# Kernel tuning notes

Measured on AMD Instinct MI355X. Metric: run time of the kernel, lower is better.

## Reference

```python
import jax, jax.numpy as jnp
import numpy as np

NEG = 0.01  # leaky_relu negative slope used throughout AttentiveFP


def _seg_softmax(logits, seg, num):
    # softmax over entries grouped by segment id (PyG softmax w/ 1e-16 eps)
    m = jax.ops.segment_max(logits, seg, num_segments=num)
    m = jnp.where(jnp.isfinite(m), m, 0.0)
    e = jnp.exp(logits - m[seg])
    s = jax.ops.segment_sum(e, seg, num_segments=num)
    return e / (s[seg] + 1e-16)


def _gru(x, h, wi, wh, bi, bh):
    # torch.nn.GRUCell math
    gi = x @ wi.T + bi
    gh = h @ wh.T + bh
    ir, iz, inn = jnp.split(gi, 3, axis=-1)
    hr, hz, hn = jnp.split(gh, 3, axis=-1)
    r = jax.nn.sigmoid(ir + hr)
    z = jax.nn.sigmoid(iz + hz)
    n = jnp.tanh(inn + r * hn)
    return (1.0 - z) * n + z * h


def _forward(x, edge_attr, mol_feats, lin1_w, lin1_b, gate_lin1_w, gate_lin2_w, gate_att_l, gate_att_r, gate_bias, grus_wi, grus_wh, grus_bi, grus_bh, atom_w, atom_att_src, atom_att_dst, atom_bias, mol_w, mol_att_src, mol_att_dst, mol_bias, lin2_w, lin2_b, fcm0_w, fcm0_b, fcm1_w, fcm1_b, fcm2_w, fcm2_b, fc0_w, fc0_b, fc1_w, fc1_b, fc2_w, fc2_b, fc3_w, fc3_b, fc4_w, fc4_b, edge_index, batch):
    N = x.shape[0]
    G = mol_feats.shape[0]
    src, dst = edge_index[0], edge_index[1]
    lrelu = lambda v: jax.nn.leaky_relu(v, NEG)
    # AttentiveFP (eval mode: dropout off)
    xh = lrelu(x @ lin1_w.T + lin1_b)  # [N,H]
    # --- GATEConv: edge-conditioned attention, add aggregation ---
    m = lrelu(jnp.concatenate([xh[src], edge_attr], axis=-1) @ gate_lin1_w.T)  # [E,H]
    a = lrelu(m @ gate_att_l + (xh @ gate_att_r)[dst])
    a = _seg_softmax(a, dst, N)
    h = jax.ops.segment_sum((m @ gate_lin2_w.T) * a[:, None], dst, num_segments=N) + gate_bias
    xh = jax.nn.relu(_gru(jax.nn.elu(h), xh, grus_wi[0], grus_wh[0], grus_bi[0], grus_bh[0]))
    # --- GATConv layers (num_layers-1 = 2, heads=1, no self loops) ---
    for l in range(2):
        xl = xh @ atom_w[l].T
        a = lrelu((xl @ atom_att_src[l])[src] + (xl @ atom_att_dst[l])[dst])
        a = _seg_softmax(a, dst, N)
        h = jax.ops.segment_sum(xl[src] * a[:, None], dst, num_segments=N) + atom_bias[l]
        xh = jax.nn.relu(_gru(jax.nn.elu(h), xh, grus_wi[1 + l], grus_wh[1 + l], grus_bi[1 + l], grus_bh[1 + l]))
    # --- attentive graph readout (num_timesteps = 3) ---
    out = jax.nn.relu(jax.ops.segment_sum(xh, batch, num_segments=G))  # [G,H]
    xm = xh @ mol_w.T            # atom-side lin (x fixed across timesteps)
    a_src = xm @ mol_att_src
    for _ in range(3):
        a = lrelu(a_src + ((out @ mol_w.T) @ mol_att_dst)[batch])
        a = _seg_softmax(a, batch, G)
        h = jax.ops.segment_sum(xm * a[:, None], batch, num_segments=G) + mol_bias
        out = jax.nn.relu(_gru(jax.nn.elu(h), out, grus_wi[3], grus_wh[3], grus_bi[3], grus_bh[3]))
    hg = out @ lin2_w.T + lin2_b  # [G,256]
    # --- mol-feature MLP branch (SiLU) ---
    hm = jax.nn.silu(mol_feats @ fcm0_w.T + fcm0_b)
    hm = jax.nn.silu(hm @ fcm1_w.T + fcm1_b)
    hm = jax.nn.silu(hm @ fcm2_w.T + fcm2_b)
    # --- fusion MLP ---
    hg = jnp.concatenate([hg, hm], axis=1)  # [G,512]
    hg = jax.nn.silu(hg @ fc0_w.T + fc0_b)
    hg = jax.nn.silu(hg @ fc1_w.T + fc1_b)
    hg = jax.nn.silu(hg @ fc2_w.T + fc2_b)
    hg = jax.nn.silu(hg @ fc3_w.T + fc3_b)
    return hg @ fc4_w.T + fc4_b  # [G,1]


def setup_inputs() -> dict:
    key = jax.random.key(0)
    ks = iter(jax.random.split(key, 64))
    def W(*shape):
        return jax.random.normal(next(ks), shape, jnp.float32) / np.float32(np.sqrt(shape[-1]))
    def B(*shape):
        return 0.02 * jax.random.normal(next(ks), shape, jnp.float32)
    N, E, G = 131072, 262144, 8192
    Fn, Fe, Fm, H = 64, 16, 200, 256
    return dict(
        x=jax.random.normal(next(ks), (N, Fn), jnp.float32),
        edge_attr=jax.random.normal(next(ks), (E, Fe), jnp.float32),
        mol_feats=jax.random.normal(next(ks), (G, Fm), jnp.float32),
        lin1_w=W(H, Fn), lin1_b=B(H),
        gate_lin1_w=W(H, H + Fe), gate_lin2_w=W(H, H),
        gate_att_l=W(H), gate_att_r=W(H), gate_bias=B(H),
        grus_wi=W(4, 3 * H, H), grus_wh=W(4, 3 * H, H), grus_bi=B(4, 3 * H), grus_bh=B(4, 3 * H),
        atom_w=W(2, H, H), atom_att_src=W(2, H), atom_att_dst=W(2, H), atom_bias=B(2, H),
        mol_w=W(H, H), mol_att_src=W(H), mol_att_dst=W(H), mol_bias=B(H),
        lin2_w=W(H, H), lin2_b=B(H),
        fcm0_w=W(H, Fm), fcm0_b=B(H), fcm1_w=W(H, H), fcm1_b=B(H), fcm2_w=W(H, H), fcm2_b=B(H),
        fc0_w=W(512, 512), fc0_b=B(512), fc1_w=W(512, 512), fc1_b=B(512),
        fc2_w=W(512, 512), fc2_b=B(512), fc3_w=W(128, 512), fc3_b=B(128),
        fc4_w=W(1, 128), fc4_b=B(1),
        edge_index=jax.random.randint(next(ks), (2, E), 0, N),
        batch=jnp.sort(jax.random.randint(next(ks), (N,), 0, G)),
    )


def reference(x, edge_attr, mol_feats, lin1_w, lin1_b, gate_lin1_w, gate_lin2_w, gate_att_l, gate_att_r, gate_bias, grus_wi, grus_wh, grus_bi, grus_bh, atom_w, atom_att_src, atom_att_dst, atom_bias, mol_w, mol_att_src, mol_att_dst, mol_bias, lin2_w, lin2_b, fcm0_w, fcm0_b, fcm1_w, fcm1_b, fcm2_w, fcm2_b, fc0_w, fc0_b, fc1_w, fc1_b, fc2_w, fc2_b, fc3_w, fc3_b, fc4_w, fc4_b, edge_index, batch):
    return _forward(x, edge_attr, mol_feats, lin1_w, lin1_b, gate_lin1_w, gate_lin2_w, gate_att_l, gate_att_r, gate_bias, grus_wi, grus_wh, grus_bi, grus_bh, atom_w, atom_att_src, atom_att_dst, atom_bias, mol_w, mol_att_src, mol_att_dst, mol_bias, lin2_w, lin2_b, fcm0_w, fcm0_b, fcm1_w, fcm1_b, fcm2_w, fcm2_b, fc0_w, fc0_b, fc1_w, fc1_b, fc2_w, fc2_b, fc3_w, fc3_b, fc4_w, fc4_b, edge_index, batch)
```

## Files before the change

### kernel.cpp

```cpp
#include <hip/hip_runtime.h>
#include <hip/hip_bf16.h>
#include <math.h>


typedef unsigned short u16;
typedef u16 u16x8 __attribute__((ext_vector_type(8)));
typedef short s16x8 __attribute__((ext_vector_type(8)));
typedef float f32x4 __attribute__((ext_vector_type(4)));

__device__ __forceinline__ float u2f(u16 u) { return __uint_as_float(((unsigned)u) << 16); }
__device__ __forceinline__ u16 f2u(float f) {
    return __builtin_bit_cast(u16, __float2bfloat16(f));
}

#define NEGS 0.01f

typedef const __attribute__((address_space(1))) unsigned gas1_t;
typedef __attribute__((address_space(3))) unsigned las3_t;
__device__ __forceinline__ void gload16(const void* g, void* l) {
    __builtin_amdgcn_global_load_lds((gas1_t*)g, (las3_t*)l, 16, 0, 0);
}

__device__ __forceinline__ unsigned fkey(float f) {
    unsigned u = __float_as_uint(f);
    return (u & 0x80000000u) ? ~u : (u | 0x80000000u);
}
__device__ __forceinline__ float funkey(unsigned k) {
    return (k & 0x80000000u) ? __uint_as_float(k ^ 0x80000000u) : __uint_as_float(~k);
}
#define KEY_NEG_INF 0x007FFFFFu

static inline int cdiv(int a, int b) { return (a + b - 1) / b; }

__global__ void fill_f32(float* p, float v, size_t n) {
    size_t i = (size_t)blockIdx.x * 256 + threadIdx.x;
    if (i < n) p[i] = v;
}
__global__ void fill_u32(unsigned* p, unsigned v, int n) {
    int i = blockIdx.x * 256 + threadIdx.x;
    if (i < n) p[i] = v;
}
__global__ void fill_km(unsigned* key, float* sum, int n) {
    int i = blockIdx.x * 256 + threadIdx.x;
    if (i < n) { key[i] = KEY_NEG_INF; sum[i] = 0.f; }
}
__global__ void copy_f2b(const float* s, u16* d, size_t n) {
    size_t i = (size_t)blockIdx.x * 256 + threadIdx.x;
    if (i < n) d[i] = f2u(s[i]);
}
__global__ void matvecT_k(const float* W, const float* a, float* v, int K, int Jout) {
    int j = blockIdx.x * 256 + threadIdx.x;
    if (j >= Jout) return;
    float s = 0.f;
    for (int k = 0; k < K; k++) s += W[(size_t)k * Jout + j] * a[k];
    v[j] = s;
}
__global__ void matvecT2_k(const float* W1, const float* a1, float* o1,
                           const float* W2, const float* a2, float* o2,
                           int K, int Jout) {
    int j = blockIdx.x * 256 + threadIdx.x;
    if (j < Jout) {
        float s = 0.f;
        for (int k = 0; k < K; k++) s += W1[(size_t)k * Jout + j] * a1[k];
        o1[j] = s;
    } else if (j < 2 * Jout) {
        int jj = j - Jout;
        float s = 0.f;
        for (int k = 0; k < K; k++) s += W2[(size_t)k * Jout + jj] * a2[k];
        o2[jj] = s;
    }
}
__global__ void edge_add_lrelu_max(const float* dp4, float* elog, const float* r,
                                   const int* dsti, unsigned* key, int E) {
    int i = blockIdx.x * 256 + threadIdx.x;
    if (i < E) {
        int d = dsti[i];
        float p = (dp4[i] + dp4[(size_t)E + i]) +
                  (dp4[(size_t)2 * E + i] + dp4[(size_t)3 * E + i]);
        float v = p + r[d];
        v = v > 0.f ? v : NEGS * v;
        elog[i] = v;
        atomicMax(&key[d], fkey(v));
    }
}
__global__ void pair_logit_max(float* elog, const float* s, const float* dd,
                               const int* srci, const int* dsti, unsigned* key, int E) {
    int i = blockIdx.x * 256 + threadIdx.x;
    if (i < E) {
        int d = dsti[i];
        float v = s[srci[i]] + dd[d];
        v = v > 0.f ? v : NEGS * v;
        elog[i] = v;
        atomicMax(&key[d], fkey(v));
    }
}
__global__ void node_logit_max(float* nlog, const float* asrc, const float* wg,
                               const int* batch, unsigned* key, int N) {
    int i = blockIdx.x * 256 + threadIdx.x;
    if (i < N) {
        int b = batch[i];
        float v = asrc[i] + wg[b];
        v = v > 0.f ? v : NEGS * v;
        nlog[i] = v;
        atomicMax(&key[b], fkey(v));
    }
}
__global__ void seg_exp_k(const float* logit, const int* idx, const unsigned* key,
                          float* ex, float* sum, int n) {
    int i = blockIdx.x * 256 + threadIdx.x;
    if (i < n) {
        float e = expf(logit[i] - funkey(key[idx[i]]));
        ex[i] = e;
        atomicAdd(&sum[idx[i]], e);
    }
}
__global__ void rowdot2_b(const u16* X, const float* v1, const float* v2,
                          float* o1, float* o2, int M) {
    int r = blockIdx.x * 4 + (threadIdx.x >> 6);
    int lane = threadIdx.x & 63;
    if (r >= M) return;
    ushort4 rv = *(const ushort4*)(X + (size_t)r * 256 + lane * 4);
    u16 q4[4] = {rv.x, rv.y, rv.z, rv.w};
    float p1 = 0.f, p2 = 0.f;
#pragma unroll
    for (int q = 0; q < 4; q++) {
        float xv = u2f(q4[q]);
        p1 += xv * v1[lane * 4 + q];
        if (v2) p2 += xv * v2[lane * 4 + q];
    }
    for (int off = 32; off; off >>= 1) {
        p1 += __shfl_down(p1, off);
        if (v2) p2 += __shfl_down(p2, off);
    }
    if (lane == 0) {
        o1[r] = p1;
        if (v2) o2[r] = p2;
    }
}
__global__ void rowdot_f(const float* X, const float* v1, float* o1, int M) {
    int r = blockIdx.x * 4 + (threadIdx.x >> 6);
    int lane = threadIdx.x & 63;
    if (r >= M) return;
    float4 a = ((const float4*)(X + (size_t)r * 256))[lane];
    float4 b = ((const float4*)v1)[lane];
    float p1 = a.x * b.x + a.y * b.y + a.z * b.z + a.w * b.w;
    for (int off = 32; off; off >>= 1) p1 += __shfl_down(p1, off);
    if (lane == 0) o1[r] = p1;
}
__global__ void fc4_k(const float* X, const float* w, const float* b, float* out, int G) {
    int g = blockIdx.x * 4 + (threadIdx.x >> 6);
    int lane = threadIdx.x & 63;
    if (g >= G) return;
    float2 xv = ((const float2*)(X + (size_t)g * 128))[lane];
    float2 wv = ((const float2*)w)[lane];
    float p = xv.x * wv.x + xv.y * wv.y;
    for (int off = 32; off; off >>= 1) p += __shfl_down(p, off);
    if (lane == 0) out[g] = p + b[0];
}

__global__ void count_dst(const int* dst, int* cnt, int E) {
    int i = blockIdx.x * 256 + threadIdx.x;
    if (i < E) atomicAdd(&cnt[dst[i]], 1);
}
__global__ void scan1(const int* cnt, int* part, int N) {
    __shared__ int sm[256];
    int i = blockIdx.x * 256 + threadIdx.x;
    sm[threadIdx.x] = i < N ? cnt[i] : 0;
    __syncthreads();
    for (int off = 128; off; off >>= 1) {
        if (threadIdx.x < off) sm[threadIdx.x] += sm[threadIdx.x + off];
        __syncthreads();
    }
    if (threadIdx.x == 0) part[blockIdx.x] = sm[0];
}
__global__ void scan2(int* part, int nb) {
    __shared__ int a[1024], b[1024];
    int t = threadIdx.x;
    if (nb > 1024) {
        if (t == 0) {
            int acc = 0;
            for (int i = 0; i < nb; i++) { int v = part[i]; part[i] = acc; acc += v; }
        }
        return;
    }
    int v = t < nb ? part[t] : 0;
    a[t] = v;
    __syncthreads();
    int* cur = a; int* nxt = b;
    for (int off = 1; off < 1024; off <<= 1) {
        int s = cur[t] + (t >= off ? cur[t - off] : 0);
        nxt[t] = s;
        __syncthreads();
        int* tmp = cur; cur = nxt; nxt = tmp;
    }
    if (t < nb) part[t] = cur[t] - v;
}
__global__ void scan3(const int* cnt, const int* part, int* rowstart, int N) {
    __shared__ int a[256], b[256];
    int t = threadIdx.x;
    int i = blockIdx.x * 256 + t;
    int v = i < N ? cnt[i] : 0;
    a[t] = v;
    __syncthreads();
    int* cur = a; int* nxt = b;
    for (int off = 1; off < 256; off <<= 1) {
        int s = cur[t] + (t >= off ? cur[t - off] : 0);
        nxt[t] = s;
        __syncthreads();
        int* tmp = cur; cur = nxt; nxt = tmp;
    }
    if (i < N) rowstart[i] = part[blockIdx.x] + cur[t] - v;
}
__global__ void fill_csr(const int* dst, const int* rowstart, int* fillc,
                         int* eorder, int E) {
    int e = blockIdx.x * 256 + threadIdx.x;
    if (e >= E) return;
    int d = dst[e];
    int s = rowstart[d] + atomicAdd(&fillc[d], 1);
    eorder[s] = e;
}
__global__ void chunk_dlo_k(const int* rowstart, const int* cnt, int N, int Crows,
                            int nch, int* dlo) {
    int c = blockIdx.x * 64 + threadIdx.x;
    if (c >= nch) return;
    int s0 = c * Crows;
    int lo = 0, hi = N;
    while (lo < hi) {
        int mid = (lo + hi) >> 1;
        if (rowstart[mid] + cnt[mid] > s0) hi = mid; else lo = mid + 1;
    }
    dlo[c] = lo;
}
template <int MODE>
__global__ void csr_red(const int* rowstart, const int* cnt, const int* eorder,
                        const float* ex, const float* sum, const int* srcE,
                        const u16* X, const u16* X2, int msplit,
                        int s0, int s1, const int* dlo,
                        u16* outH, u16* outL, int N) {
    int d;
    if (MODE == 1) {
        d = dlo[0] + blockIdx.x;
        if (d >= N) return;
        if (rowstart[d] >= s1) return;
    } else {
        d = blockIdx.x;
        if (d >= N) return;
    }
    int rs = rowstart[d], k = cnt[d];
    int lo = rs, hi = rs + k;
    if (MODE == 1) {
        if (lo < s0) lo = s0;
        if (hi > s1) hi = s1;
        if (lo >= hi) return;
    }
    float den = sum[d] + 1e-16f;
    int c = threadIdx.x;
    float acc = 0.f;
    for (int s = lo; s < hi; s++) {
        int e = eorder[s];
        float av = ex[e] / den;
        const u16* row;
        if (MODE == 0) row = X + (size_t)srcE[e] * 256;
        else if (MODE == 1) row = X + (size_t)(s - s0) * 256;
        else row = (e < msplit) ? X + (size_t)e * 256 : X2 + (size_t)(e - msplit) * 256;
        acc += av * u2f(row[c]);
    }
    size_t o = (size_t)d * 256 + c;
    if (MODE == 1) acc += u2f(outH[o]) + u2f(outL[o]);
    u16 hh = f2u(acc);
    outH[o] = hh;
    outL[o] = f2u(acc - u2f(hh));
}
__global__ void graph_bounds(const int* batch, int* gs, int* ge, int N) {
    int i = blockIdx.x * 256 + threadIdx.x;
    if (i >= N) return;
    int b = batch[i];
    atomicMin(&gs[b], i);
    atomicMax(&ge[b], i + 1);
}
template <bool RELU>
__global__ void seg_red(const int* gs, const int* ge, const u16* X, const float* sc,
                        const float* sum, float* out, int G) {
    int g = blockIdx.x;
    if (g >= G) return;
    int c = threadIdx.x;
    int s = gs[g], e = ge[g];
    float den = sc ? (sum[g] + 1e-16f) : 1.f;
    float acc = 0.f;
    if (s < e)
        for (int i = s; i < e; i++) {
            float v = u2f(X[(size_t)i * 256 + c]);
            if (sc) v *= sc[i] / den;
            acc += v;
        }
    out[(size_t)g * 256 + c] = RELU ? fmaxf(acc, 0.f) : acc;
}

__global__ void pack_w(const float* s1, const float* s2, int K1, int Ksrc,
                       int Nout, int Kp, u16* dst) {
    int idx = blockIdx.x * 256 + threadIdx.x;
    int kiters = Kp >> 5;
    int total = (Nout >> 7) * kiters * 512;
    if (idx >= total) return;
    int c = idx & 511;
    int rest = idx >> 9;
    int ki = rest % kiters, nb = rest / kiters;
    int n = (nb << 7) + (((c >> 6) & 7) << 4) + (c & 15);
    int k0 = (ki << 5) + (((c >> 4) & 3) << 3);
    u16x8 vh, vl;
#pragma unroll
    for (int j = 0; j < 8; j++) {
        int k = k0 + j;
        float f = 0.f;
        if (k < K1) f = s1[(size_t)n * K1 + k];
        else if (k < Ksrc) f = s2[(size_t)n * (Ksrc - K1) + (k - K1)];
        u16 h = f2u(f);
        vh[j] = h;
        vl[j] = f2u(f - u2f(h));
    }
    ((u16x8*)dst)[idx] = vh;
    ((u16x8*)dst)[idx + total] = vl;
}
__global__ void pack_gru_w(const float* wi, const float* wh, u16* dst) {
    int idx = blockIdx.x * 256 + threadIdx.x;
    const int total = 8 * 16 * 512;
    if (idx >= total) return;
    int c = idx & 511, rest = idx >> 9;
    int ki = rest & 15, nb = rest >> 4;
    int n = (nb << 7) + (((c >> 6) & 7) << 4) + (c & 15);
    int k0 = (ki << 5) + (((c >> 4) & 3) << 3);
    int grp = n >> 6, sub = (n >> 4) & 3, ch = grp * 16 + (n & 15);
    u16x8 vh, vl;
#pragma unroll
    for (int j = 0; j < 8; j++) {
        int k = k0 + j;
        float f;
        if (sub < 3) {
            int srow = sub * 256 + ch;
            f = (k < 256) ? wi[(size_t)srow * 256 + k]
                          : wh[(size_t)srow * 256 + (k - 256)];
        } else {
            f = (k < 256) ? 0.f : wh[(size_t)(512 + ch) * 256 + (k - 256)];
        }
        u16 h = f2u(f);
        vh[j] = h;
        vl[j] = f2u(f - u2f(h));
    }
    ((u16x8*)dst)[idx] = vh;
    ((u16x8*)dst)[idx + total] = vl;
}
__global__ void pack_gru_b(const float* bi, const float* bh, float* bp) {
    int n = blockIdx.x * 256 + threadIdx.x;
    if (n >= 1024) return;
    int grp = n >> 6, sub = (n >> 4) & 3, ch = grp * 16 + (n & 15);
    float v;
    if (sub == 0) v = bi[ch] + bh[ch];
    else if (sub == 1) v = bi[256 + ch] + bh[256 + ch];
    else if (sub == 2) v = bi[512 + ch] + bh[512 + ch];
    else v = bh[512 + ch];
    bp[n] = v;
}

struct p8 { u16x8 hi, lo; };
__device__ __forceinline__ u16x8 zero8() {
    u16x8 z;
#pragma unroll
    for (int j = 0; j < 8; j++) z[j] = 0;
    return z;
}
__device__ __forceinline__ p8 sp_zero() { p8 r; r.hi = zero8(); r.lo = zero8(); return r; }
__device__ __forceinline__ p8 sp_b(const u16* p) {
    p8 r;
    r.hi = *(const u16x8*)p;
    r.lo = zero8();
    return r;
}
__device__ __forceinline__ p8 sp_f(const float* p) {
    p8 r;
#pragma unroll
    for (int j = 0; j < 8; j++) {
        float x = p[j];
        u16 h = f2u(x);
        r.hi[j] = h;
        r.lo[j] = f2u(x - u2f(h));
    }
    return r;
}
__device__ __forceinline__ p8 sp_eluf(const float* p) {
    p8 r;
#pragma unroll
    for (int j = 0; j < 8; j++) {
        float x = p[j];
        float e = x > 0.f ? x : expm1f(x);
        u16 h = f2u(e);
        r.hi[j] = h;
        r.lo[j] = f2u(e - u2f(h));
    }
    return r;
}
template <int ALD>
__device__ __forceinline__ p8 ldA(bool valid, int k, int Ksrc, const u16* ab,
                                  const float* af, const float* x2) {
    if (!valid) return sp_zero();
    if (ALD == 1) {
        if (k >= Ksrc) return sp_zero();
        return sp_f(af + k);
    }
    if (ALD == 2 || ALD == 7) {
        if (k < 256) return sp_b(ab + k);
        if (k < 272) return sp_f(x2 + (k - 256));
        return sp_zero();
    }
    if (k < 256) return sp_eluf(af + k);
    return sp_f(x2 + (k - 256));
}
template <int ALD>
__device__ __forceinline__ bool lo_zero(int ki) {
    if (ALD == 2 || ALD == 7) return ki < 8;
    return false;
}
template <int ACT>
__device__ __forceinline__ float actf(float v) {
    if (ACT == 1) return v > 0.f ? v : NEGS * v;
    if (ACT == 3) return v / (1.f + expf(-v));
    return v;
}

template <int ALD, int ACT, int EPI>
__global__ __launch_bounds__(256, 4) void mgemm(
    int M, int Kp, int Ksrc,
    const float* Af, int lda, const u16* Ab, const u16* Ab2,
    const int* gidx, const float* X2f, const u16* Wp, const float* b1,
    float* Cf, u16* Cb, u16* Cb2, int csplit, int ldc,
    const float* attv, float* dotout, const int* didx) {
    __shared__ u16x8 lsAll[2048];
    u16x8* lsAh = lsAll;
    u16x8* lsAl = lsAll + 512;
    u16x8* lsWh = lsAll + 1024;
    u16x8* lsWl = lsAll + 1536;
    const int t = threadIdx.x;
    const int m0 = blockIdx.x * 128;
    const int nb = blockIdx.y;
    const int kiters = Kp >> 5;
    const int r0 = ((t >> 6) << 4) | (t & 15);
    const int kq = ((t >> 4) & 3) << 3;
    const int mA[2] = {m0 + r0, m0 + r0 + 64};
    const u16* abh[2]; const u16* abl[2];
    const float* afr[2]; const float* x2r[2];
    bool val[2];
#pragma unroll
    for (int h = 0; h < 2; h++) {
        int m = mA[h];
        val[h] = (m < M);
        int ms = val[h] ? m : 0;
        abh[h] = nullptr; abl[h] = nullptr; afr[h] = nullptr; x2r[h] = nullptr;
        if constexpr (ALD == 1) {
            afr[h] = Af + (size_t)ms * lda;
        } else if constexpr (ALD == 2) {
            abh[h] = Ab + (size_t)gidx[ms] * 256;
            x2r[h] = X2f + (size_t)ms * 16;
        } else if constexpr (ALD == 7) {
            int e = gidx[ms];
            abh[h] = Ab + (size_t)didx[e] * 256;
            x2r[h] = X2f + (size_t)e * 16;
        } else {
            abh[h] = Ab + (size_t)ms * 256;
            abl[h] = Ab2 + (size_t)ms * 256;
        }
    }
    const int wave = t >> 6, lane = t & 63;
    const int wm = (wave >> 1) << 6, wn = (wave & 1) << 6;
    f32x4 acc[4][4];
#pragma unroll
    for (int i = 0; i < 4; i++)
#pragma unroll
        for (int j = 0; j < 4; j++) {
            acc[i][j][0] = 0.f; acc[i][j][1] = 0.f; acc[i][j][2] = 0.f; acc[i][j][3] = 0.f;
        }
    const u16x8* wh0 = (const u16x8*)Wp + ((size_t)nb * kiters << 9);
    const u16x8* wl0 = wh0 + ((size_t)gridDim.y * kiters << 9);
    for (int ki = 0; ki < kiters; ki++) {
        int kb = (ki << 5) + kq;
        if constexpr (ALD == 6) {
            gload16(abh[0] + kb, &lsAh[t]);
            gload16(abh[1] + kb, &lsAh[t + 256]);
            gload16(abl[0] + kb, &lsAl[t]);
            gload16(abl[1] + kb, &lsAl[t + 256]);
        } else {
            p8 a0 = ldA<ALD>(val[0], kb, Ksrc, abh[0], afr[0], x2r[0]);
            p8 a1 = ldA<ALD>(val[1], kb, Ksrc, abh[1], afr[1], x2r[1]);
            lsAh[t] = a0.hi; lsAl[t] = a0.lo;
            lsAh[t + 256] = a1.hi; lsAl[t + 256] = a1.lo;
        }
        const u16x8* wsh = wh0 + ((size_t)ki << 9);
        const u16x8* wsl = wl0 + ((size_t)ki << 9);
        gload16(wsh + t, &lsWh[t]);
        gload16(wsh + t + 256, &lsWh[t + 256]);
        gload16(wsl + t, &lsWl[t]);
        gload16(wsl + t + 256, &lsWl[t + 256]);
        __syncthreads();
        s16x8 ah[4], al[4], wh[4], wl[4];
#pragma unroll
        for (int f = 0; f < 4; f++) {
            int ai = ((wm >> 4) + f) * 64 + lane;
            int wi = ((wn >> 4) + f) * 64 + lane;
            ah[f] = __builtin_bit_cast(s16x8, lsAh[ai]);
            al[f] = __builtin_bit_cast(s16x8, lsAl[ai]);
            wh[f] = __builtin_bit_cast(s16x8, lsWh[wi]);
            wl[f] = __builtin_bit_cast(s16x8, lsWl[wi]);
        }
        bool skip_lh = lo_zero<ALD>(ki);
#pragma unroll
        for (int fi = 0; fi < 4; fi++)
#pragma unroll
            for (int fj = 0; fj < 4; fj++) {
                acc[fi][fj] = __builtin_amdgcn_mfma_f32_16x16x32_bf16(
                    ah[fi], wh[fj], acc[fi][fj], 0, 0, 0);
                if (!skip_lh)
                    acc[fi][fj] = __builtin_amdgcn_mfma_f32_16x16x32_bf16(
                        al[fi], wh[fj], acc[fi][fj], 0, 0, 0);
                acc[fi][fj] = __builtin_amdgcn_mfma_f32_16x16x32_bf16(
                    ah[fi], wl[fj], acc[fi][fj], 0, 0, 0);
            }
        __syncthreads();
    }
    const int col = lane & 15, quad = lane >> 4;
    const int n_base = nb * 128 + wn;
    u16* lt = (u16*)lsAll;
    const int rowsM = M - m0;
    if constexpr (EPI == 2) {
        float dp[4][4] = {};
#pragma unroll
        for (int fi = 0; fi < 4; fi++)
#pragma unroll
            for (int fj = 0; fj < 4; fj++) {
                int nn = n_base + fj * 16 + col;
                float av = attv[nn];
#pragma unroll
                for (int r = 0; r < 4; r++) {
                    float v = actf<ACT>(acc[fi][fj][r]);
                    dp[fi][r] += v * av;
                    if (Cb) {
                        int lr = wm + fi * 16 + quad * 4 + r;
                        int lc = wn + fj * 16 + col;
                        lt[lr * 128 + lc] = f2u(v);
                    }
                }
            }
        const size_t slot = (size_t)(nb * 2 + (wn >> 6)) * (size_t)M;
#pragma unroll
        for (int fi = 0; fi < 4; fi++)
#pragma unroll
            for (int r = 0; r < 4; r++) {
                float p = dp[fi][r];
                p += __shfl_down(p, 8);
                p += __shfl_down(p, 4);
                p += __shfl_down(p, 2);
                p += __shfl_down(p, 1);
                int mm = m0 + wm + fi * 16 + quad * 4 + r;
                if (col == 0 && mm < M) dotout[slot + mm] = p;
            }
        if (Cb) {
            __syncthreads();
#pragma unroll
            for (int it = 0; it < 8; it++) {
                int idx = it * 256 + t;
                int row = idx >> 4, c8 = idx & 15;
                if (row < rowsM) {
                    int mm = m0 + row;
                    u16* dst = (mm < csplit) ? Cb + (size_t)mm * 256
                                             : Cb2 + (size_t)(mm - csplit) * 256;
                    ((u16x8*)(dst + nb * 128))[c8] = ((u16x8*)lt)[idx];
                }
            }
        }
    } else if constexpr (EPI == 4) {
#pragma unroll
        for (int fj = 0; fj < 4; fj++) {
            int nn = n_base + fj * 16 + col;
            float bb = b1 ? b1[nn] : 0.f;
#pragma unroll
            for (int fi = 0; fi < 4; fi++)
#pragma unroll
                for (int r = 0; r < 4; r++) {
                    float v = acc[fi][fj][r] + bb;
                    float e = v > 0.f ? v : expm1f(v);
                    int lr = wm + fi * 16 + quad * 4 + r;
                    int lc = wn + fj * 16 + col;
                    lt[lr * 128 + lc] = f2u(e);
                }
        }
        __syncthreads();
#pragma unroll
        for (int it = 0; it < 8; it++) {
            int idx = it * 256 + t;
            int row = idx >> 4, c8 = idx & 15;
            if (row < rowsM)
                ((u16x8*)(Cb + (size_t)(m0 + row) * ldc + nb * 128))[c8] =
                    ((u16x8*)lt)[idx];
        }
        __syncthreads();
#pragma unroll
        for (int fj = 0; fj < 4; fj++) {
            int nn = n_base + fj * 16 + col;
            float bb = b1 ? b1[nn] : 0.f;
#pragma unroll
            for (int fi = 0; fi < 4; fi++)
#pragma unroll
                for (int r = 0; r < 4; r++) {
                    float v = acc[fi][fj][r] + bb;
                    float e = v > 0.f ? v : expm1f(v);
                    u16 hh = f2u(e);
                    int lr = wm + fi * 16 + quad * 4 + r;
                    int lc = wn + fj * 16 + col;
                    lt[lr * 128 + lc] = f2u(e - u2f(hh));
                }
        }
        __syncthreads();
#pragma unroll
        for (int it = 0; it < 8; it++) {
            int idx = it * 256 + t;
            int row = idx >> 4, c8 = idx & 15;
            if (row < rowsM)
                ((u16x8*)(Cb2 + (size_t)(m0 + row) * ldc + nb * 128))[c8] =
                    ((u16x8*)lt)[idx];
        }
    } else if constexpr (EPI == 1) {
#pragma unroll
        for (int fj = 0; fj < 4; fj++) {
            int nn = n_base + fj * 16 + col;
            float bb = b1 ? b1[nn] : 0.f;
#pragma unroll
            for (int fi = 0; fi < 4; fi++)
#pragma unroll
                for (int r = 0; r < 4; r++) {
                    float v = actf<ACT>(acc[fi][fj][r] + bb);
                    int lr = wm + fi * 16 + quad * 4 + r;
                    int lc = wn + fj * 16 + col;
                    lt[lr * 128 + lc] = f2u(v);
                }
        }
        __syncthreads();
#pragma unroll
        for (int it = 0; it < 8; it++) {
            int idx = it * 256 + t;
            int row = idx >> 4, c8 = idx & 15;
            if (row < rowsM)
                ((u16x8*)(Cb + (size_t)(m0 + row) * ldc + nb * 128))[c8] =
                    ((u16x8*)lt)[idx];
        }
    } else {
#pragma unroll
        for (int fj = 0; fj < 4; fj++) {
            int nn = n_base + fj * 16 + col;
            float bb = b1 ? b1[nn] : 0.f;
#pragma unroll
            for (int fi = 0; fi < 4; fi++)
#pragma unroll
                for (int r = 0; r < 4; r++) {
                    int mm = m0 + wm + fi * 16 + quad * 4 + r;
                    if (mm >= M) continue;
                    float v = actf<ACT>(acc[fi][fj][r] + bb);
                    Cf[(size_t)mm * ldc + nn] = v;
                }
        }
    }
}

template <int ALD, bool HB, bool OB>
__global__ __launch_bounds__(256, 4) void mgemm_gru(
    int M, const float* Af, const u16* Ab, const u16* Ab2, const float* X2f,
    const u16* Wp, const float* bp, const u16* hb, const float* hf,
    float* of, u16* ob) {
    __shared__ u16x8 lsAll[2048];
    u16x8* lsAh = lsAll;
    u16x8* lsAl = lsAll + 512;
    u16x8* lsWh = lsAll + 1024;
    u16x8* lsWl = lsAll + 1536;
    const int t = threadIdx.x;
    const int m0 = blockIdx.x * 128;
    const int nb = blockIdx.y;
    const int r0 = ((t >> 6) << 4) | (t & 15);
    const int kq = ((t >> 4) & 3) << 3;
    const int mA[2] = {m0 + r0, m0 + r0 + 64};
    const u16* ehr[2]; const u16* elr[2]; const u16* xhr[2];
    const float* afr[2]; const float* x2r[2];
    bool val[2];
#pragma unroll
    for (int h = 0; h < 2; h++) {
        int m = mA[h];
        val[h] = (m < M);
        int ms = val[h] ? m : 0;
        ehr[h] = nullptr; elr[h] = nullptr; xhr[h] = nullptr;
        afr[h] = nullptr; x2r[h] = nullptr;
        if constexpr (ALD == 5) {
            ehr[h] = Ab + (size_t)ms * 256;
            elr[h] = Ab2 + (size_t)ms * 256;
            xhr[h] = hb + (size_t)ms * 256;
        } else {
            afr[h] = Af + (size_t)ms * 256;
            x2r[h] = X2f + (size_t)ms * 256;
        }
    }
    const int wave = t >> 6, lane = t & 63;
    const int wm = (wave >> 1) << 6, wn = (wave & 1) << 6;
    f32x4 acc[4][4];
#pragma unroll
    for (int i = 0; i < 4; i++)
#pragma unroll
        for (int j = 0; j < 4; j++) {
            acc[i][j][0] = 0.f; acc[i][j][1] = 0.f; acc[i][j][2] = 0.f; acc[i][j][3] = 0.f;
        }
    const u16x8* wh0 = (const u16x8*)Wp + ((size_t)nb * 16 << 9);
    const u16x8* wl0 = (const u16x8*)Wp + (size_t)(8 * 16 * 512) + ((size_t)nb * 16 << 9);
    for (int ki = 0; ki < 16; ki++) {
        int kb = (ki << 5) + kq;
        if constexpr (ALD == 5) {
            const u16* p0 = kb < 256 ? ehr[0] + kb : xhr[0] + (kb - 256);
            const u16* p1 = kb < 256 ? ehr[1] + kb : xhr[1] + (kb - 256);
            gload16(p0, &lsAh[t]);
            gload16(p1, &lsAh[t + 256]);
            if (ki < 8) {
                gload16(elr[0] + kb, &lsAl[t]);
                gload16(elr[1] + kb, &lsAl[t + 256]);
            }
        } else {
            p8 a0 = ldA<4>(val[0], kb, 512, nullptr, afr[0], x2r[0]);
            p8 a1 = ldA<4>(val[1], kb, 512, nullptr, afr[1], x2r[1]);
            lsAh[t] = a0.hi; lsAl[t] = a0.lo;
            lsAh[t + 256] = a1.hi; lsAl[t + 256] = a1.lo;
        }
        const u16x8* wsh = wh0 + ((size_t)ki << 9);
        const u16x8* wsl = wl0 + ((size_t)ki << 9);
        gload16(wsh + t, &lsWh[t]);
        gload16(wsh + t + 256, &lsWh[t + 256]);
        gload16(wsl + t, &lsWl[t]);
        gload16(wsl + t + 256, &lsWl[t + 256]);
        __syncthreads();
        s16x8 ah[4], al[4], wh[4], wl[4];
#pragma unroll
        for (int f = 0; f < 4; f++) {
            int ai = ((wm >> 4) + f) * 64 + lane;
            int wi = ((wn >> 4) + f) * 64 + lane;
            ah[f] = __builtin_bit_cast(s16x8, lsAh[ai]);
            al[f] = __builtin_bit_cast(s16x8, lsAl[ai]);
            wh[f] = __builtin_bit_cast(s16x8, lsWh[wi]);
            wl[f] = __builtin_bit_cast(s16x8, lsWl[wi]);
        }
        bool skip_lh = (ALD == 5) ? (ki >= 8) : false;
        bool hn_zero = (ki < 8);
#pragma unroll
        for (int fi = 0; fi < 4; fi++)
#pragma unroll
            for (int fj = 0; fj < 4; fj++) {
                if (fj == 3 && hn_zero) continue;
                acc[fi][fj] = __builtin_amdgcn_mfma_f32_16x16x32_bf16(
                    ah[fi], wh[fj], acc[fi][fj], 0, 0, 0);
                if (!skip_lh)
                    acc[fi][fj] = __builtin_amdgcn_mfma_f32_16x16x32_bf16(
                        al[fi], wh[fj], acc[fi][fj], 0, 0, 0);
                acc[fi][fj] = __builtin_amdgcn_mfma_f32_16x16x32_bf16(
                    ah[fi], wl[fj], acc[fi][fj], 0, 0, 0);
            }
        __syncthreads();
    }
    const int col = lane & 15, quad = lane >> 4;
    const int nbase = nb * 128 + wn;
    float br = bp[nbase + col];
    float bz = bp[nbase + 16 + col];
    float bn = bp[nbase + 32 + col];
    float bhn = bp[nbase + 48 + col];
    int ch = (nb * 2 + (wn >> 6)) * 16 + col;
    int lc = ((wn >> 6) << 4) + col;
    u16* lt = (u16*)lsAll;
    float* ft = (float*)lsAll;
#pragma unroll
    for (int fi = 0; fi < 4; fi++)
#pragma unroll
        for (int r = 0; r < 4; r++) {
            int m = m0 + wm + fi * 16 + quad * 4 + r;
            if (m >= M) continue;
            float rs = acc[fi][0][r] + br;
            float zs = acc[fi][1][r] + bz;
            float nsv = acc[fi][2][r] + bn;
            float hnv = acc[fi][3][r] + bhn;
            float rr = 1.f / (1.f + expf(-rs));
            float zz = 1.f / (1.f + expf(-zs));
            float nn = tanhf(nsv - hnv + rr * hnv);
            float ho = HB ? u2f(hb[(size_t)m * 256 + ch]) : hf[(size_t)m * 256 + ch];
            float o = fmaxf((1.f - zz) * nn + zz * ho, 0.f);
            int lr = wm + fi * 16 + quad * 4 + r;
            if (OB) lt[lr * 32 + lc] = f2u(o);
            else ft[lr * 32 + lc] = o;
        }
    __syncthreads();
    const int rowsM = M - m0;
    if (OB) {
#pragma unroll
        for (int it = 0; it < 2; it++) {
            int idx = it * 256 + t;
            int row = idx >> 2, c8 = idx & 3;
            if (row < rowsM)
                ((u16x8*)(ob + (size_t)(m0 + row) * 256 + nb * 32))[c8] =
                    ((u16x8*)lt)[idx];
        }
    } else {
#pragma unroll
        for (int it = 0; it < 4; it++) {
            int idx = it * 256 + t;
            int row = idx >> 3, c4 = idx & 7;
            if (row < rowsM)
                ((float4*)(of + (size_t)(m0 + row) * 256 + nb * 32))[c4] =
                    ((float4*)ft)[idx];
        }
    }
}

extern "C" void kernel_launch(void* const* d_in, const int* in_sizes, int n_in,
                              void* d_out, int out_size, void* d_ws, size_t ws_size,
                              hipStream_t stream) {
    const float* x = (const float*)d_in[0];
    const float* edge_attr = (const float*)d_in[1];
    const float* mol_feats = (const float*)d_in[2];
    const float* lin1_w = (const float*)d_in[3];
    const float* lin1_b = (const float*)d_in[4];
    const float* gate_lin1_w = (const float*)d_in[5];
    const float* gate_lin2_w = (const float*)d_in[6];
    const float* gate_att_l = (const float*)d_in[7];
    const float* gate_att_r = (const float*)d_in[8];
    const float* gate_bias = (const float*)d_in[9];
    const float* grus_wi = (const float*)d_in[10];
    const float* grus_wh = (const float*)d_in[11];
    const float* grus_bi = (const float*)d_in[12];
    const float* grus_bh = (const float*)d_in[13];
    const float* atom_w = (const float*)d_in[14];
    const float* atom_att_src = (const float*)d_in[15];
    const float* atom_att_dst = (const float*)d_in[16];
    const float* atom_bias = (const float*)d_in[17];
    const float* mol_w = (const float*)d_in[18];
    const float* mol_att_src = (const float*)d_in[19];
    const float* mol_att_dst = (const float*)d_in[20];
    const float* mol_bias = (const float*)d_in[21];
    const float* lin2_w = (const float*)d_in[22];
    const float* lin2_b = (const float*)d_in[23];
    const float* fcm0_w = (const float*)d_in[24];
    const float* fcm0_b = (const float*)d_in[25];
    const float* fcm1_w = (const float*)d_in[26];
    const float* fcm1_b = (const float*)d_in[27];
    const float* fcm2_w = (const float*)d_in[28];
    const float* fcm2_b = (const float*)d_in[29];
    const float* fc0_w = (const float*)d_in[30];
    const float* fc0_b = (const float*)d_in[31];
    const float* fc1_w = (const float*)d_in[32];
    const float* fc1_b = (const float*)d_in[33];
    const float* fc2_w = (const float*)d_in[34];
    const float* fc2_b = (const float*)d_in[35];
    const float* fc3_w = (const float*)d_in[36];
    const float* fc3_b = (const float*)d_in[37];
    const float* fc4_w = (const float*)d_in[38];
    const float* fc4_b = (const float*)d_in[39];
    const int* edge_index = (const int*)d_in[40];
    const int* batch = (const int*)d_in[41];
    float* out_final = (float*)d_out;

    const int N = in_sizes[0] / 64;
    const int E = in_sizes[1] / 16;
    const int G = in_sizes[2] / 200;
    const int* srcE = edge_index;
    const int* dstE = edge_index + E;

    char* base = (char*)d_ws;
    size_t off = 0;
    auto alloc = [&](size_t bytes) -> char* {
        char* p = base + off;
        off += (bytes + 255) & ~(size_t)255;
        return p;
    };
    u16* xhA = (u16*)alloc((size_t)N * 512);
    u16* haggH = (u16*)alloc((size_t)N * 512);
    u16* haggL = (u16*)alloc((size_t)N * 512);
    float* outg = (float*)alloc((size_t)G * 1024);
    float* hgrb = (float*)alloc((size_t)G * 1024);
    float* elog = (float*)alloc((size_t)E * 4);
    float* eexp = (float*)alloc((size_t)E * 4);
    float* dotp = (float*)alloc((size_t)E * 16);
    unsigned* nkey = (unsigned*)alloc((size_t)N * 4);
    float* nsum = (float*)alloc((size_t)N * 4);
    float* ns1 = (float*)alloc((size_t)N * 4);
    float* ns2 = (float*)alloc((size_t)N * 4);
    unsigned* gkey = (unsigned*)alloc((size_t)G * 4);
    float* gsum = (float*)alloc((size_t)G * 4);
    float* wgb = (float*)alloc((size_t)G * 4);
    float* vbuf = (float*)alloc(4096);
    int* ecnt = (int*)alloc((size_t)N * 4);
    int* efill = (int*)alloc((size_t)N * 4);
    int* erowst = (int*)alloc((size_t)N * 4);
    int* eorder = (int*)alloc((size_t)E * 4);
    int* spart = (int*)alloc(4096 * 4);
    int* cdlo = (int*)alloc(((size_t)E / 128 + 2) * 4);
    int* gs = (int*)alloc((size_t)G * 4);
    int* ge = (int*)alloc((size_t)G * 4);
    u16* pk_lin1 = (u16*)alloc(256 * 64 * 2 * 2);
    u16* pk_g1 = (u16*)alloc(256 * 288 * 2 * 2);
    u16* pk_g2 = (u16*)alloc(256 * 256 * 2 * 2);
    u16* pk_gruF[4];
    float* bp_gru[4];
    for (int l = 0; l < 4; l++) {
        pk_gruF[l] = (u16*)alloc(1024 * 512 * 2 * 2);
        bp_gru[l] = (float*)alloc(1024 * 4);
    }
    u16* pk_atom[2];
    for (int l = 0; l < 2; l++) pk_atom[l] = (u16*)alloc(256 * 256 * 2 * 2);
    u16* pk_mol = (u16*)alloc(256 * 256 * 2 * 2);
    u16* pk_lin2 = (u16*)alloc(256 * 256 * 2 * 2);
    u16* pk_fcm0 = (u16*)alloc(256 * 224 * 2 * 2);
    u16* pk_fcm1 = (u16*)alloc(256 * 256 * 2 * 2);
    u16* pk_fcm2 = (u16*)alloc(256 * 256 * 2 * 2);
    u16* pk_fc0 = (u16*)alloc(512 * 512 * 2 * 2);
    u16* pk_fc1 = (u16*)alloc(512 * 512 * 2 * 2);
    u16* pk_fc2 = (u16*)alloc(512 * 512 * 2 * 2);
    u16* pk_fc3 = (u16*)alloc(128 * 512 * 2 * 2);
    size_t fixed_core = off;
    if (fixed_core + (size_t)2 * 1024 * 1024 > ws_size) {
        fill_f32<<<cdiv(out_size, 256), 256, 0, stream>>>(out_final, (float)ws_size,
                                                          (size_t)out_size);
        return;
    }
    u16* xhB = nullptr;
    bool use_pp = false;
    if (ws_size - off >= (size_t)N * 512 + (size_t)2 * 1024 * 1024) {
        xhB = (u16*)alloc((size_t)N * 512);
        use_pp = true;
    }
    size_t workbytes = ws_size - off;
    char* workp = base + off;
    int Mc = (int)((workbytes / (use_pp ? 1024 : 2048)) & ~(size_t)127);
    if (Mc > N) Mc = N;
    if (Mc < 128) Mc = 128;
    u16* ehi = (u16*)workp;
    u16* elo = ehi + (size_t)Mc * 256;
    float* htmp = (float*)(workp + (size_t)Mc * 1024);
    float* cbuf = (float*)workp;
    u16* mt1 = nullptr; u16* mt2 = nullptr; int msplit = 0x7fffffff;
    if (workbytes >= (size_t)E * 512) { mt1 = (u16*)workp; msplit = E; }
    else if (use_pp) {
        if (N >= E) { mt1 = xhB; msplit = E; }
        else if ((size_t)N * 512 + workbytes >= (size_t)E * 512) {
            mt1 = xhB; msplit = N; mt2 = (u16*)workp;
        }
    }
    bool gate_store = (mt1 != nullptr);
    size_t crows_sz = workbytes / 512;
    if (crows_sz > (size_t)E) crows_sz = (size_t)E;
    int Crows = (int)(crows_sz & ~(size_t)127);
    if (Crows < 128) Crows = 128;
    int nch = cdiv(E, Crows);
    u16* mchunk = (u16*)workp;
    float* fbufA = (float*)haggH;
    float* fbufB = fbufA + (size_t)G * 512;
    float* fbufC = fbufB + (size_t)G * 512;
    float* f128 = fbufC + (size_t)G * 512;
    float* hm1 = f128 + (size_t)G * 128;
    float* hm2 = hm1 + (size_t)G * 256;

    auto pack = [&](const float* s1, const float* s2, int K1, int Ksrc, int Nout,
                    int Kp, u16* dst) {
        int total = (Nout >> 7) * (Kp >> 5) * 512;
        pack_w<<<cdiv(total, 256), 256, 0, stream>>>(s1, s2, K1, Ksrc, Nout, Kp, dst);
    };
    pack(lin1_w, nullptr, 64, 64, 256, 64, pk_lin1);
    pack(gate_lin1_w, nullptr, 272, 272, 256, 288, pk_g1);
    pack(gate_lin2_w, nullptr, 256, 256, 256, 256, pk_g2);
    for (int l = 0; l < 4; l++) {
        pack_gru_w<<<cdiv(8 * 16 * 512, 256), 256, 0, stream>>>(
            grus_wi + (size_t)l * 768 * 256, grus_wh + (size_t)l * 768 * 256,
            pk_gruF[l]);
        pack_gru_b<<<4, 256, 0, stream>>>(grus_bi + (size_t)l * 768,
                                          grus_bh + (size_t)l * 768, bp_gru[l]);
    }
    for (int l = 0; l < 2; l++)
        pack(atom_w + (size_t)l * 256 * 256, nullptr, 256, 256, 256, 256, pk_atom[l]);
    pack(mol_w, nullptr, 256, 256, 256, 256, pk_mol);
    pack(lin2_w, nullptr, 256, 256, 256, 256, pk_lin2);
    pack(fcm0_w, nullptr, 200, 200, 256, 224, pk_fcm0);
    pack(fcm1_w, nullptr, 256, 256, 256, 256, pk_fcm1);
    pack(fcm2_w, nullptr, 256, 256, 256, 256, pk_fcm2);
    pack(fc0_w, nullptr, 512, 512, 512, 512, pk_fc0);
    pack(fc1_w, nullptr, 512, 512, 512, 512, pk_fc1);
    pack(fc2_w, nullptr, 512, 512, 512, 512, pk_fc2);
    pack(fc3_w, nullptr, 512, 512, 128, 512, pk_fc3);

    int nbk = cdiv(N, 256);
    fill_u32<<<nbk, 256, 0, stream>>>((unsigned*)ecnt, 0u, N);
    fill_u32<<<nbk, 256, 0, stream>>>((unsigned*)efill, 0u, N);
    count_dst<<<cdiv(E, 256), 256, 0, stream>>>(dstE, ecnt, E);
    scan1<<<nbk, 256, 0, stream>>>(ecnt, spart, N);
    scan2<<<1, 1024, 0, stream>>>(spart, nbk);
    scan3<<<nbk, 256, 0, stream>>>(ecnt, spart, erowst, N);
    fill_csr<<<cdiv(E, 256), 256, 0, stream>>>(dstE, erowst, efill, eorder, E);
    fill_u32<<<cdiv(G, 256), 256, 0, stream>>>((unsigned*)gs, (unsigned)N, G);
    fill_u32<<<cdiv(G, 256), 256, 0, stream>>>((unsigned*)ge, 0u, G);
    graph_bounds<<<nbk, 256, 0, stream>>>(batch, gs, ge, N);

    u16* xh_cur = xhA;
    u16* xh_nxt = xhB;

    auto node_gru = [&](int l, const u16* Wpre, const float* bpre) {
        for (int c0 = 0; c0 < N; c0 += Mc) {
            int Ms = N - c0 < Mc ? N - c0 : Mc;
            int gx = cdiv(Ms, 128);
            mgemm<6, 0, 4><<<dim3(gx, 2), 256, 0, stream>>>(Ms, 256, 256,
                nullptr, 0, haggH + (size_t)c0 * 256, haggL + (size_t)c0 * 256,
                nullptr, nullptr, Wpre, bpre,
                nullptr, ehi, elo, 0, 256, nullptr, nullptr, nullptr);
            if (use_pp) {
                mgemm_gru<5, true, true><<<dim3(gx, 8), 256, 0, stream>>>(Ms,
                    nullptr, ehi, elo, nullptr, pk_gruF[l], bp_gru[l],
                    xh_cur + (size_t)c0 * 256, nullptr,
                    nullptr, xh_nxt + (size_t)c0 * 256);
            } else {
                mgemm_gru<5, true, false><<<dim3(gx, 8), 256, 0, stream>>>(Ms,
                    nullptr, ehi, elo, nullptr, pk_gruF[l], bp_gru[l],
                    xh_cur + (size_t)c0 * 256, nullptr,
                    htmp, nullptr);
                copy_f2b<<<(int)(((size_t)Ms * 256 + 255) / 256), 256, 0, stream>>>(
                    htmp, xh_cur + (size_t)c0 * 256, (size_t)Ms * 256);
            }
        }
        if (use_pp) { u16* t2 = xh_cur; xh_cur = xh_nxt; xh_nxt = t2; }
    };

    mgemm<1, 1, 1><<<dim3(cdiv(N, 128), 2), 256, 0, stream>>>(N, 64, 64,
        x, 64, nullptr, nullptr, nullptr, nullptr, pk_lin1, lin1_b,
        nullptr, xh_cur, nullptr, 0, 256, nullptr, nullptr, nullptr);

    mgemm<2, 1, 2><<<dim3(cdiv(E, 128), 2), 256, 0, stream>>>(E, 288, 272,
        nullptr, 0, xh_cur, nullptr, srcE, edge_attr, pk_g1, nullptr,
        nullptr, gate_store ? mt1 : nullptr, mt2, msplit, 256,
        gate_att_l, dotp, nullptr);
    rowdot2_b<<<cdiv(N, 4), 256, 0, stream>>>(xh_cur, gate_att_r, nullptr, ns1, nullptr, N);
    fill_km<<<nbk, 256, 0, stream>>>(nkey, nsum, N);
    edge_add_lrelu_max<<<cdiv(E, 256), 256, 0, stream>>>(dotp, elog, ns1, dstE, nkey, E);
    seg_exp_k<<<cdiv(E, 256), 256, 0, stream>>>(elog, dstE, nkey, eexp, nsum, E);
    if (gate_store) {
        csr_red<2><<<N, 256, 0, stream>>>(erowst, ecnt, eorder, eexp, nsum, nullptr,
            mt1, mt2, msplit, 0, E, nullptr, haggH, haggL, N);
    } else {
        fill_u32<<<cdiv(N * 256, 256), 256, 0, stream>>>((unsigned*)haggH, 0u, N * 256);
        chunk_dlo_k<<<cdiv(nch, 64), 64, 0, stream>>>(erowst, ecnt, N, Crows, nch, cdlo);
        for (int c = 0; c < nch; c++) {
            int s0 = c * Crows;
            int s1 = s0 + Crows < E ? s0 + Crows : E;
            int Ms = s1 - s0;
            mgemm<7, 1, 1><<<dim3(cdiv(Ms, 128), 2), 256, 0, stream>>>(Ms, 288, 272,
                nullptr, 0, xh_cur, nullptr, eorder + s0, edge_attr, pk_g1, nullptr,
                nullptr, mchunk, nullptr, 0x7fffffff, 256,
                nullptr, nullptr, srcE);
            csr_red<1><<<Crows, 256, 0, stream>>>(erowst, ecnt, eorder, eexp, nsum,
                nullptr, mchunk, nullptr, 0, s0, s1, cdlo + c, haggH, haggL, N);
        }
    }
    node_gru(0, pk_g2, gate_bias);

    for (int l = 0; l < 2; l++) {
        const float* aw = atom_w + (size_t)l * 256 * 256;
        matvecT2_k<<<2, 256, 0, stream>>>(aw, atom_att_src + (size_t)l * 256, vbuf,
                                          aw, atom_att_dst + (size_t)l * 256, vbuf + 256,
                                          256, 256);
        rowdot2_b<<<cdiv(N, 4), 256, 0, stream>>>(xh_cur, vbuf, vbuf + 256, ns1, ns2, N);
        fill_km<<<nbk, 256, 0, stream>>>(nkey, nsum, N);
        pair_logit_max<<<cdiv(E, 256), 256, 0, stream>>>(elog, ns1, ns2, srcE, dstE, nkey, E);
        seg_exp_k<<<cdiv(E, 256), 256, 0, stream>>>(elog, dstE, nkey, eexp, nsum, E);
        csr_red<0><<<N, 256, 0, stream>>>(erowst, ecnt, eorder, eexp, nsum, srcE,
            xh_cur, nullptr, 0, 0, 0, nullptr, haggH, haggL, N);
        node_gru(1 + l, pk_atom[l], atom_bias + (size_t)l * 256);
    }

    seg_red<true><<<G, 256, 0, stream>>>(gs, ge, xh_cur, nullptr, nullptr, outg, G);
    matvecT2_k<<<2, 256, 0, stream>>>(mol_w, mol_att_dst, vbuf,
                                      mol_w, mol_att_src, vbuf + 256, 256, 256);
    rowdot2_b<<<cdiv(N, 4), 256, 0, stream>>>(xh_cur, vbuf + 256, nullptr, ns1, nullptr, N);
    float* ogc = outg;
    float* ogn = hgrb;
    int McG = Mc < G ? Mc : G;
    for (int t = 0; t < 3; t++) {
        rowdot_f<<<cdiv(G, 4), 256, 0, stream>>>(ogc, vbuf, wgb, G);
        fill_km<<<cdiv(G, 256), 256, 0, stream>>>(gkey, gsum, G);
        node_logit_max<<<nbk, 256, 0, stream>>>(elog, ns1, wgb, batch, gkey, N);
        seg_exp_k<<<nbk, 256, 0, stream>>>(elog, batch, gkey, eexp, gsum, N);
        seg_red<false><<<G, 256, 0, stream>>>(gs, ge, xh_cur, eexp, gsum, ogn, G);
        for (int c0 = 0; c0 < G; c0 += McG) {
            int Ms = G - c0 < McG ? G - c0 : McG;
            int gx = cdiv(Ms, 128);
            mgemm<1, 0, 0><<<dim3(gx, 2), 256, 0, stream>>>(Ms, 256, 256,
                ogn + (size_t)c0 * 256, 256, nullptr, nullptr, nullptr, nullptr,
                pk_mol, mol_bias, cbuf, nullptr, nullptr, 0, 256,
                nullptr, nullptr, nullptr);
            mgemm_gru<4, false, false><<<dim3(gx, 8), 256, 0, stream>>>(Ms,
                cbuf, nullptr, nullptr, ogc + (size_t)c0 * 256, pk_gruF[3], bp_gru[3],
                nullptr, ogc + (size_t)c0 * 256, ogn + (size_t)c0 * 256, nullptr);
        }
        float* tt = ogc; ogc = ogn; ogn = tt;
    }

    int gG = cdiv(G, 128);
    mgemm<1, 0, 0><<<dim3(gG, 2), 256, 0, stream>>>(G, 256, 256, ogc, 256,
        nullptr, nullptr, nullptr, nullptr, pk_lin2, lin2_b,
        fbufA, nullptr, nullptr, 0, 512, nullptr, nullptr, nullptr);
    mgemm<1, 3, 0><<<dim3(gG, 2), 256, 0, stream>>>(G, 224, 200, mol_feats, 200,
        nullptr, nullptr, nullptr, nullptr, pk_fcm0, fcm0_b,
        hm1, nullptr, nullptr, 0, 256, nullptr, nullptr, nullptr);
    mgemm<1, 3, 0><<<dim3(gG, 2), 256, 0, stream>>>(G, 256, 256, hm1, 256,
        nullptr, nullptr, nullptr, nullptr, pk_fcm1, fcm1_b,
        hm2, nullptr, nullptr, 0, 256, nullptr, nullptr, nullptr);
    mgemm<1, 3, 0><<<dim3(gG, 2), 256, 0, stream>>>(G, 256, 256, hm2, 256,
        nullptr, nullptr, nullptr, nullptr, pk_fcm2, fcm2_b,
        fbufA + 256, nullptr, nullptr, 0, 512, nullptr, nullptr, nullptr);
    mgemm<1, 3, 0><<<dim3(gG, 4), 256, 0, stream>>>(G, 512, 512, fbufA, 512,
        nullptr, nullptr, nullptr, nullptr, pk_fc0, fc0_b,
        fbufB, nullptr, nullptr, 0, 512, nullptr, nullptr, nullptr);
    mgemm<1, 3, 0><<<dim3(gG, 4), 256, 0, stream>>>(G, 512, 512, fbufB, 512,
        nullptr, nullptr, nullptr, nullptr, pk_fc1, fc1_b,
        fbufC, nullptr, nullptr, 0, 512, nullptr, nullptr, nullptr);
    mgemm<1, 3, 0><<<dim3(gG, 4), 256, 0, stream>>>(G, 512, 512, fbufC, 512,
        nullptr, nullptr, nullptr, nullptr, pk_fc2, fc2_b,
        fbufB, nullptr, nullptr, 0, 512, nullptr, nullptr, nullptr);
    mgemm<1, 3, 0><<<dim3(gG, 1), 256, 0, stream>>>(G, 512, 512, fbufB, 512,
        nullptr, nullptr, nullptr, nullptr, pk_fc3, fc3_b,
        f128, nullptr, nullptr, 0, 128, nullptr, nullptr, nullptr);
    fc4_k<<<cdiv(G, 4), 256, 0, stream>>>(f128, fc4_w, fc4_b, out_final, G);
}
```

Before: 5.434 ms.

## Fuse softmax exp and sum into segment reduction kernels, stage dot outputs in LDS

Removes the separate seg_exp kernel and its atomic sum buffer. The CSR and graph reduction kernels now recompute the exponentials and the denominator per destination from the logits and max key. This cuts one launch and the atomicAdd traffic per attention stage, but each block repeats the exp work per row (every thread recomputes the sum). The mgemm EPI==2 epilogue also stages its per-row dot products in LDS so they can be written out with coalesced stores.

```diff
diff --git a/kernel.cpp b/kernel.cpp
--- a/kernel.cpp
+++ b/kernel.cpp
@@ -40,20 +40,9 @@
     int i = blockIdx.x * 256 + threadIdx.x;
     if (i < n) p[i] = v;
 }
-__global__ void fill_km(unsigned* key, float* sum, int n) {
-    int i = blockIdx.x * 256 + threadIdx.x;
-    if (i < n) { key[i] = KEY_NEG_INF; sum[i] = 0.f; }
-}
 __global__ void copy_f2b(const float* s, u16* d, size_t n) {
     size_t i = (size_t)blockIdx.x * 256 + threadIdx.x;
     if (i < n) d[i] = f2u(s[i]);
-}
-__global__ void matvecT_k(const float* W, const float* a, float* v, int K, int Jout) {
-    int j = blockIdx.x * 256 + threadIdx.x;
-    if (j >= Jout) return;
-    float s = 0.f;
-    for (int k = 0; k < K; k++) s += W[(size_t)k * Jout + j] * a[k];
-    v[j] = s;
 }
 __global__ void matvecT2_k(const float* W1, const float* a1, float* o1,
                            const float* W2, const float* a2, float* o2,
@@ -105,15 +94,6 @@
         atomicMax(&key[b], fkey(v));
     }
 }
-__global__ void seg_exp_k(const float* logit, const int* idx, const unsigned* key,
-                          float* ex, float* sum, int n) {
-    int i = blockIdx.x * 256 + threadIdx.x;
-    if (i < n) {
-        float e = expf(logit[i] - funkey(key[idx[i]]));
-        ex[i] = e;
-        atomicAdd(&sum[idx[i]], e);
-    }
-}
 __global__ void rowdot2_b(const u16* X, const float* v1, const float* v2,
                           float* o1, float* o2, int M) {
     int r = blockIdx.x * 4 + (threadIdx.x >> 6);
@@ -233,7 +213,7 @@
 }
 template <int MODE>
 __global__ void csr_red(const int* rowstart, const int* cnt, const int* eorder,
-                        const float* ex, const float* sum, const int* srcE,
+                        const float* elog, const unsigned* key, const int* srcE,
                         const u16* X, const u16* X2, int msplit,
                         int s0, int s1, const int* dlo,
                         u16* outH, u16* outL, int N) {
@@ -253,12 +233,15 @@
         if (hi > s1) hi = s1;
         if (lo >= hi) return;
     }
-    float den = sum[d] + 1e-16f;
+    float mx = funkey(key[d]);
+    float dsum = 0.f;
+    for (int s = rs; s < rs + k; s++) dsum += expf(elog[eorder[s]] - mx);
+    float den = dsum + 1e-16f;
     int c = threadIdx.x;
     float acc = 0.f;
     for (int s = lo; s < hi; s++) {
         int e = eorder[s];
-        float av = ex[e] / den;
+        float av = expf(elog[e] - mx) / den;
         const u16* row;
         if (MODE == 0) row = X + (size_t)srcE[e] * 256;
         else if (MODE == 1) row = X + (size_t)(s - s0) * 256;
@@ -279,18 +262,25 @@
     atomicMax(&ge[b], i + 1);
 }
 template <bool RELU>
-__global__ void seg_red(const int* gs, const int* ge, const u16* X, const float* sc,
-                        const float* sum, float* out, int G) {
+__global__ void seg_red(const int* gs, const int* ge, const u16* X, const float* elog,
+                        const unsigned* key, float* out, int G) {
     int g = blockIdx.x;
     if (g >= G) return;
     int c = threadIdx.x;
     int s = gs[g], e = ge[g];
-    float den = sc ? (sum[g] + 1e-16f) : 1.f;
+    float mx = 0.f, den = 1.f;
+    if (elog) {
+        mx = funkey(key[g]);
+        float dsum = 0.f;
+        if (s < e)
+            for (int i = s; i < e; i++) dsum += expf(elog[i] - mx);
+        den = dsum + 1e-16f;
+    }
     float acc = 0.f;
     if (s < e)
         for (int i = s; i < e; i++) {
             float v = u2f(X[(size_t)i * 256 + c]);
-            if (sc) v *= sc[i] / den;
+            if (elog) v *= expf(elog[i] - mx) / den;
             acc += v;
         }
     out[(size_t)g * 256 + c] = RELU ? fmaxf(acc, 0.f) : acc;
@@ -433,7 +423,7 @@
     const int* gidx, const float* X2f, const u16* Wp, const float* b1,
     float* Cf, u16* Cb, u16* Cb2, int csplit, int ldc,
     const float* attv, float* dotout, const int* didx) {
-    __shared__ u16x8 lsAll[2048];
+    __shared__ u16x8 lsAll[2112];
     u16x8* lsAh = lsAll;
     u16x8* lsAl = lsAll + 512;
     u16x8* lsWh = lsAll + 1024;
@@ -529,6 +519,7 @@
     u16* lt = (u16*)lsAll;
     const int rowsM = M - m0;
     if constexpr (EPI == 2) {
+        float* dpb = (float*)(lsAll + 2048);
         float dp[4][4] = {};
 #pragma unroll
         for (int fi = 0; fi < 4; fi++)
@@ -547,7 +538,6 @@
                     }
                 }
             }
-        const size_t slot = (size_t)(nb * 2 + (wn >> 6)) * (size_t)M;
 #pragma unroll
         for (int fi = 0; fi < 4; fi++)
 #pragma unroll
@@ -557,11 +547,17 @@
                 p += __shfl_down(p, 4);
                 p += __shfl_down(p, 2);
                 p += __shfl_down(p, 1);
-                int mm = m0 + wm + fi * 16 + quad * 4 + r;
-                if (col == 0 && mm < M) dotout[slot + mm] = p;
+                if (col == 0)
+                    dpb[((wn >> 6) << 7) + wm + fi * 16 + quad * 4 + r] = p;
             }
+        __syncthreads();
+        {
+            int row = t & 127, sl = t >> 7;
+            if (row < rowsM)
+                dotout[(size_t)(nb * 2 + sl) * (size_t)M + m0 + row] =
+                    dpb[sl * 128 + row];
+        }
         if (Cb) {
-            __syncthreads();
 #pragma unroll
             for (int it = 0; it < 8; it++) {
                 int idx = it * 256 + t;
@@ -882,14 +878,11 @@
     float* outg = (float*)alloc((size_t)G * 1024);
     float* hgrb = (float*)alloc((size_t)G * 1024);
     float* elog = (float*)alloc((size_t)E * 4);
-    float* eexp = (float*)alloc((size_t)E * 4);
     float* dotp = (float*)alloc((size_t)E * 16);
     unsigned* nkey = (unsigned*)alloc((size_t)N * 4);
-    float* nsum = (float*)alloc((size_t)N * 4);
     float* ns1 = (float*)alloc((size_t)N * 4);
     float* ns2 = (float*)alloc((size_t)N * 4);
     unsigned* gkey = (unsigned*)alloc((size_t)G * 4);
-    float* gsum = (float*)alloc((size_t)G * 4);
     float* wgb = (float*)alloc((size_t)G * 4);
     float* vbuf = (float*)alloc(4096);
     int* ecnt = (int*)alloc((size_t)N * 4);
@@ -1039,11 +1032,10 @@
         nullptr, gate_store ? mt1 : nullptr, mt2, msplit, 256,
         gate_att_l, dotp, nullptr);
     rowdot2_b<<<cdiv(N, 4), 256, 0, stream>>>(xh_cur, gate_att_r, nullptr, ns1, nullptr, N);
-    fill_km<<<nbk, 256, 0, stream>>>(nkey, nsum, N);
+    fill_u32<<<nbk, 256, 0, stream>>>(nkey, KEY_NEG_INF, N);
     edge_add_lrelu_max<<<cdiv(E, 256), 256, 0, stream>>>(dotp, elog, ns1, dstE, nkey, E);
-    seg_exp_k<<<cdiv(E, 256), 256, 0, stream>>>(elog, dstE, nkey, eexp, nsum, E);
     if (gate_store) {
-        csr_red<2><<<N, 256, 0, stream>>>(erowst, ecnt, eorder, eexp, nsum, nullptr,
+        csr_red<2><<<N, 256, 0, stream>>>(erowst, ecnt, eorder, elog, nkey, nullptr,
             mt1, mt2, msplit, 0, E, nullptr, haggH, haggL, N);
     } else {
         fill_u32<<<cdiv(N * 256, 256), 256, 0, stream>>>((unsigned*)haggH, 0u, N * 256);
@@ -1056,7 +1048,7 @@
                 nullptr, 0, xh_cur, nullptr, eorder + s0, edge_attr, pk_g1, nullptr,
                 nullptr, mchunk, nullptr, 0x7fffffff, 256,
                 nullptr, nullptr, srcE);
-            csr_red<1><<<Crows, 256, 0, stream>>>(erowst, ecnt, eorder, eexp, nsum,
+            csr_red<1><<<Crows, 256, 0, stream>>>(erowst, ecnt, eorder, elog, nkey,
                 nullptr, mchunk, nullptr, 0, s0, s1, cdlo + c, haggH, haggL, N);
         }
     }
@@ -1068,10 +1060,9 @@
                                           aw, atom_att_dst + (size_t)l * 256, vbuf + 256,
                                           256, 256);
         rowdot2_b<<<cdiv(N, 4), 256, 0, stream>>>(xh_cur, vbuf, vbuf + 256, ns1, ns2, N);
-        fill_km<<<nbk, 256, 0, stream>>>(nkey, nsum, N);
+        fill_u32<<<nbk, 256, 0, stream>>>(nkey, KEY_NEG_INF, N);
         pair_logit_max<<<cdiv(E, 256), 256, 0, stream>>>(elog, ns1, ns2, srcE, dstE, nkey, E);
-        seg_exp_k<<<cdiv(E, 256), 256, 0, stream>>>(elog, dstE, nkey, eexp, nsum, E);
-        csr_red<0><<<N, 256, 0, stream>>>(erowst, ecnt, eorder, eexp, nsum, srcE,
+        csr_red<0><<<N, 256, 0, stream>>>(erowst, ecnt, eorder, elog, nkey, srcE,
             xh_cur, nullptr, 0, 0, 0, nullptr, haggH, haggL, N);
         node_gru(1 + l, pk_atom[l], atom_bias + (size_t)l * 256);
     }
@@ -1085,10 +1076,9 @@
     int McG = Mc < G ? Mc : G;
     for (int t = 0; t < 3; t++) {
         rowdot_f<<<cdiv(G, 4), 256, 0, stream>>>(ogc, vbuf, wgb, G);
-        fill_km<<<cdiv(G, 256), 256, 0, stream>>>(gkey, gsum, G);
+        fill_u32<<<cdiv(G, 256), 256, 0, stream>>>(gkey, KEY_NEG_INF, G);
         node_logit_max<<<nbk, 256, 0, stream>>>(elog, ns1, wgb, batch, gkey, N);
-        seg_exp_k<<<nbk, 256, 0, stream>>>(elog, batch, gkey, eexp, gsum, N);
-        seg_red<false><<<G, 256, 0, stream>>>(gs, ge, xh_cur, eexp, gsum, ogn, G);
+        seg_red<false><<<G, 256, 0, stream>>>(gs, ge, xh_cur, elog, gkey, ogn, G);
         for (int c0 = 0; c0 < G; c0 += McG) {
             int Ms = G - c0 < McG ? G - c0 : McG;
             int gx = cdiv(Ms, 128);
```

Result: slower. 5.787 ms (+6.5%).
